# Kernel optimization log

Measured on AMD Instinct MI355X. Metric: run time of the kernel, lower is better.

The kernel has to match this reference:

```python
import jax, jax.numpy as jnp
import numpy as np

NUM_MAPS = 512
NUM_BLOCKS = 2
ZG = 512
HID = min(96, NUM_MAPS)          # shared query / attention hidden dim
SEQ = 8                           # hardcoded inner sequence length
H1 = min(NUM_MAPS // 32, 3)       # num_heads1 = 3
H2 = NUM_MAPS // 32               # num_heads2 = 16
NPROC = NUM_BLOCKS * 4            # 4 FiLM param types per block


def _mha(q, k, v, nheads):
    """Multi-head attention. q:(Lq,D) k,v:(Lk,D) -> (Lq,D)."""
    Lq, D = q.shape
    Lk = k.shape[0]
    d = D // nheads
    qh = q.reshape(Lq, nheads, d).transpose(1, 0, 2)   # (h,Lq,d)
    kh = k.reshape(Lk, nheads, d).transpose(1, 0, 2)
    vh = v.reshape(Lk, nheads, d).transpose(1, 0, 2)
    A = jax.nn.softmax(jnp.einsum('hqd,hkd->hqk', qh, kh) / jnp.sqrt(jnp.asarray(D, q.dtype)))
    O = jnp.einsum('hqk,hkd->hqd', A, vh)
    return O.transpose(1, 0, 2).reshape(Lq, D)


def setup_inputs() -> dict:
    key = jax.random.key(0)
    ks = jax.random.split(key, 20)
    s = 0.05
    n = jax.random.normal
    return {
        'gate': jax.random.uniform(ks[0], (1, SEQ), dtype=jnp.float32),
        'x': n(ks[1], (1, ZG), dtype=jnp.float32),
        # shared_layer_alphaC : Linear(ZG, NUM_MAPS) + Sigmoid
        'Wa': n(ks[2], (ZG, NUM_MAPS)) * s, 'ba': jnp.zeros((NUM_MAPS,)),
        # shared_layer_Query : Linear(ZG, HID) + ReLU
        'Wqr': n(ks[3], (ZG, HID)) * s, 'bqr': jnp.zeros((HID,)),
        # stacked FiLM params: [block, {g1,b1,g2,b2}, num_maps, 8]
        'P': n(ks[4], (NUM_BLOCKS, 4, NUM_MAPS, SEQ)) * 0.2,
        'De': n(ks[5], (NUM_BLOCKS, 4, NUM_MAPS, SEQ)) * 0.01,
        'regs': n(ks[6], (NUM_BLOCKS, 4, NUM_MAPS)) * 0.001,
        # SMAB_small processor weights, stacked over the 8 processors
        'Wq1': n(ks[7], (NPROC, NUM_MAPS, HID)) * s,
        'Wk1': n(ks[8], (NPROC, NUM_MAPS, HID)) * s,
        'Wv1': n(ks[9], (NPROC, NUM_MAPS, HID)) * s,
        'fc1': n(ks[10], (NPROC, HID, HID)) * s,
        'Wq2': n(ks[11], (NPROC, HID, HID)) * s,
        'Wk2': n(ks[12], (NPROC, HID, HID)) * s,
        'Wv2': n(ks[13], (NPROC, HID, HID)) * s,
        'fc2': n(ks[14], (NPROC, HID, HID)) * s,
        'Wo': n(ks[15], (NPROC, HID, NUM_MAPS)) * s,
    }


def reference(gate, x, Wa, ba, Wqr, bqr, P, De, regs,
              Wq1, Wk1, Wv1, fc1, Wq2, Wk2, Wv2, fc2, Wo):
    alpha = jax.nn.sigmoid(x @ Wa + ba).reshape(-1)        # (NUM_MAPS,)
    q = jax.nn.relu(x @ Wqr + bqr)                          # (1, HID)

    # per-processor key/value set: transpose(1,0).view(1,8,num_maps)
    K_all = P.reshape(NPROC, NUM_MAPS, SEQ).transpose(0, 2, 1)  # (8procs, 8, NUM_MAPS)

    def smab(K, wq1, wk1, wv1, f1, wq2, wk2, wv2, f2, wo):
        # stage 1: self-attention over the 8-element set (num_heads1)
        Qk = K @ wq1                                        # (8, HID)
        H = Qk + _mha(Qk, K @ wk1, K @ wv1, H1)
        H = H + jax.nn.relu(H @ f1)
        # stage 2: task query attends to the set (num_heads2)
        Qq = q @ wq2                                        # (1, HID)
        O = Qq + _mha(Qq, H @ wk2, H @ wv2, H2)
        O = O + jax.nn.relu(O @ f2)
        return (O @ wo)[0]                                  # (NUM_MAPS,)

    trans = jax.vmap(smab)(K_all, Wq1, Wk1, Wv1, fc1, Wq2, Wk2, Wv2, fc2, Wo)
    trans = trans.reshape(NUM_BLOCKS, 4, NUM_MAPS)

    de = (De * gate[0]).sum(-1)                             # (NB,4,NUM_MAPS)
    mix = alpha * trans + (1.0 - alpha) * de
    offs = jnp.array([1.0, 0.0, 1.0, 0.0], dtype=mix.dtype).reshape(1, 4, 1)
    # gamma gets +1 offset, beta does not
    return mix * regs + offs
```

## Files before the change

kernel.cpp:

```cpp
#include <hip/hip_runtime.h>
#include <hip/hip_bf16.h>
#include <math.h>


#define WS_ALPHA 0
#define WS_Q     512
#define WS_QKV   608

__global__ __launch_bounds__(256) void k1_qkv_alpha_q(
    const float* __restrict__ x, const float* __restrict__ Wa,
    const float* __restrict__ ba, const float* __restrict__ Wqr,
    const float* __restrict__ bqr, const float* __restrict__ P,
    const float* __restrict__ Wq1, const float* __restrict__ Wk1,
    const float* __restrict__ Wv1, float* __restrict__ ws)
{
    __shared__ float sK[8 * 512];
    __shared__ float sp[256];
    const int blk = blockIdx.x, tid = threadIdx.x;

    if (blk < 288) {
        const int proc = blk / 36, c = blk % 36;
        const float4* P4 = (const float4*)(P + proc * 4096);
        for (int i = tid; i < 1024; i += 256) {
            float4 v = P4[i];
            const int m = i >> 1, off = (i & 1) * 4;
            sK[(off + 0) * 512 + m] = v.x;
            sK[(off + 1) * 512 + m] = v.y;
            sK[(off + 2) * 512 + m] = v.z;
            sK[(off + 3) * 512 + m] = v.w;
        }
        __syncthreads();
        const int rl = tid & 63, qtr = tid >> 6;
        const int r = c * 64 + rl;
        const int mat = r / 768, r2 = r % 768;
        const int s = r2 / 96, h = r2 % 96;
        const float* W = (mat == 0 ? Wq1 : (mat == 1 ? Wk1 : Wv1))
                         + proc * 49152 + (qtr * 128) * 96 + h;
        const float* Ks = sK + s * 512 + qtr * 128;
        float acc = 0.f;
        #pragma unroll 32
        for (int m = 0; m < 128; ++m) acc += Ks[m] * W[m * 96];
        sp[tid] = acc;
        __syncthreads();
        if (qtr == 0) {
            acc = sp[tid] + sp[tid + 64] + sp[tid + 128] + sp[tid + 192];
            ws[WS_QKV + proc * 2304 + r] = acc;
        }
    } else if (blk < 296) {
        for (int k = tid; k < 512; k += 256) sK[k] = x[k];
        __syncthreads();
        const int ml = tid & 63, qtr = tid >> 6;
        const int m = (blk - 288) * 64 + ml;
        const float* W = Wa + (qtr * 128) * 512 + m;
        const float* xq = sK + qtr * 128;
        float acc = 0.f;
        #pragma unroll 32
        for (int k = 0; k < 128; ++k) acc += xq[k] * W[k * 512];
        sp[tid] = acc;
        __syncthreads();
        if (qtr == 0) {
            acc = sp[tid] + sp[tid + 64] + sp[tid + 128] + sp[tid + 192] + ba[m];
            ws[WS_ALPHA + m] = 1.f / (1.f + __expf(-acc));
        }
    } else {
        for (int k = tid; k < 512; k += 256) sK[k] = x[k];
        __syncthreads();
        const int hl = tid & 63, qtr = tid >> 6;
        const int h = (blk - 296) * 64 + hl;
        float acc = 0.f;
        if (h < 96) {
            const float* W = Wqr + (qtr * 128) * 96 + h;
            const float* xq = sK + qtr * 128;
            #pragma unroll 32
            for (int k = 0; k < 128; ++k) acc += xq[k] * W[k * 96];
        }
        sp[tid] = acc;
        __syncthreads();
        if (qtr == 0 && h < 96) {
            acc = sp[tid] + sp[tid + 64] + sp[tid + 128] + sp[tid + 192] + bqr[h];
            ws[WS_Q + h] = fmaxf(acc, 0.f);
        }
    }
}

__global__ __launch_bounds__(512) void k2_attn_out(
    const float* __restrict__ gate, const float* __restrict__ De,
    const float* __restrict__ regs, const float* __restrict__ fc1,
    const float* __restrict__ Wq2, const float* __restrict__ Wk2,
    const float* __restrict__ Wv2, const float* __restrict__ fc2,
    const float* __restrict__ Wo, const float* __restrict__ ws,
    float* __restrict__ out)
{
    const int proc = blockIdx.x, tid = threadIdx.x;
    __shared__ float sQk[768], sKk[768], sVv[768], sH[768], sH2[768];
    __shared__ float sK2[768], sV2[768];
    __shared__ float sq[96], sQq[96], sO[96], sOf[96], sS[192], sg[8];
    const float rs = 0.10206207261596577f;

    const float* qkv = ws + WS_QKV + proc * 2304;
    for (int i = tid; i < 768; i += 512) {
        sQk[i] = qkv[i]; sKk[i] = qkv[768 + i]; sVv[i] = qkv[1536 + i];
    }
    if (tid < 96) sq[tid] = ws[WS_Q + tid];
    if (tid < 8)  sg[tid] = gate[tid];
    __syncthreads();

    if (tid < 192) {
        const int h0 = tid / 64, rem = tid % 64, si = rem / 8, sk = rem % 8;
        float acc = 0.f;
        #pragma unroll
        for (int d = 0; d < 32; ++d)
            acc += sQk[si * 96 + h0 * 32 + d] * sKk[sk * 96 + h0 * 32 + d];
        sS[tid] = acc * rs;
    }
    __syncthreads();

    if (tid < 24) {
        const int h0 = tid / 8, si = tid % 8;
        const float* row = sS + h0 * 64 + si * 8;
        float mx = row[0];
        #pragma unroll
        for (int k = 1; k < 8; ++k) mx = fmaxf(mx, row[k]);
        float e[8], sum = 0.f;
        #pragma unroll
        for (int k = 0; k < 8; ++k) { e[k] = __expf(row[k] - mx); sum += e[k]; }
        const float inv = 1.f / sum;
        #pragma unroll
        for (int d = 0; d < 32; ++d) {
            float o = 0.f;
            #pragma unroll
            for (int k = 0; k < 8; ++k) o += e[k] * sVv[k * 96 + h0 * 32 + d];
            const int idx = si * 96 + h0 * 32 + d;
            sH[idx] = sQk[idx] + o * inv;
        }
    }
    __syncthreads();

    for (int idx = tid; idx < 768; idx += 512) {
        const int s = idx / 96, j = idx % 96;
        const float* W = fc1 + proc * 9216 + j;
        const float* Hs = sH + s * 96;
        float acc = 0.f;
        #pragma unroll 32
        for (int i = 0; i < 96; ++i) acc += Hs[i] * W[i * 96];
        sH2[idx] = sH[idx] + fmaxf(acc, 0.f);
    }
    if (tid < 96) {
        const float* W = Wq2 + proc * 9216 + tid;
        float acc = 0.f;
        #pragma unroll 32
        for (int i = 0; i < 96; ++i) acc += sq[i] * W[i * 96];
        sQq[tid] = acc;
    }
    __syncthreads();

    for (int idx = tid; idx < 1536; idx += 512) {
        const int which = idx / 768, r = idx % 768;
        const int s = r / 96, j = r % 96;
        const float* W = (which ? Wv2 : Wk2) + proc * 9216 + j;
        const float* Hs = sH2 + s * 96;
        float acc = 0.f;
        #pragma unroll 32
        for (int i = 0; i < 96; ++i) acc += Hs[i] * W[i * 96];
        if (which) sV2[r] = acc; else sK2[r] = acc;
    }
    __syncthreads();

    if (tid < 16) {
        const int h0 = tid;
        float lg[8], mx = -1e30f;
        #pragma unroll
        for (int k = 0; k < 8; ++k) {
            float acc = 0.f;
            #pragma unroll
            for (int d = 0; d < 6; ++d)
                acc += sQq[h0 * 6 + d] * sK2[k * 96 + h0 * 6 + d];
            lg[k] = acc * rs; mx = fmaxf(mx, lg[k]);
        }
        float e[8], sum = 0.f;
        #pragma unroll
        for (int k = 0; k < 8; ++k) { e[k] = __expf(lg[k] - mx); sum += e[k]; }
        const float inv = 1.f / sum;
        #pragma unroll
        for (int d = 0; d < 6; ++d) {
            float o = 0.f;
            #pragma unroll
            for (int k = 0; k < 8; ++k) o += e[k] * sV2[k * 96 + h0 * 6 + d];
            sO[h0 * 6 + d] = sQq[h0 * 6 + d] + o * inv;
        }
    }
    __syncthreads();

    if (tid < 96) {
        const float* W = fc2 + proc * 9216 + tid;
        float acc = 0.f;
        #pragma unroll 32
        for (int i = 0; i < 96; ++i) acc += sO[i] * W[i * 96];
        sOf[tid] = sO[tid] + fmaxf(acc, 0.f);
    }
    __syncthreads();

    {
        const int m = tid;
        const float* W = Wo + proc * 49152 + m;
        float tr = 0.f;
        #pragma unroll 32
        for (int h = 0; h < 96; ++h) tr += sOf[h] * W[h * 512];
        const float* Dp = De + proc * 4096 + m * 8;
        float de = 0.f;
        #pragma unroll
        for (int s = 0; s < 8; ++s) de += Dp[s] * sg[s];
        const float a = ws[WS_ALPHA + m];
        const float mix = a * tr + (1.f - a) * de;
        const int pt = proc & 3;
        const float off = (pt == 0 || pt == 2) ? 1.f : 0.f;
        out[proc * 512 + m] = mix * regs[proc * 512 + m] + off;
    }
}

extern "C" void kernel_launch(void* const* d_in, const int* in_sizes, int n_in,
                              void* d_out, int out_size, void* d_ws, size_t ws_size,
                              hipStream_t stream)
{
    const float* gate = (const float*)d_in[0];
    const float* x    = (const float*)d_in[1];
    const float* Wa   = (const float*)d_in[2];
    const float* ba   = (const float*)d_in[3];
    const float* Wqr  = (const float*)d_in[4];
    const float* bqr  = (const float*)d_in[5];
    const float* P    = (const float*)d_in[6];
    const float* De   = (const float*)d_in[7];
    const float* regs = (const float*)d_in[8];
    const float* Wq1  = (const float*)d_in[9];
    const float* Wk1  = (const float*)d_in[10];
    const float* Wv1  = (const float*)d_in[11];
    const float* fc1  = (const float*)d_in[12];
    const float* Wq2  = (const float*)d_in[13];
    const float* Wk2  = (const float*)d_in[14];
    const float* Wv2  = (const float*)d_in[15];
    const float* fc2  = (const float*)d_in[16];
    const float* Wo   = (const float*)d_in[17];
    float* ws = (float*)d_ws;

    hipLaunchKernelGGL(k1_qkv_alpha_q, dim3(298), dim3(256), 0, stream,
                       x, Wa, ba, Wqr, bqr, P, Wq1, Wk1, Wv1, ws);
    hipLaunchKernelGGL(k2_attn_out, dim3(8), dim3(512), 0, stream,
                       gate, De, regs, fc1, Wq2, Wk2, Wv2, fc2, Wo, ws,
                       (float*)d_out);
}
```

Measured before the change: 116.6 us.

## Double k1 grid with 8-way K split and prefetch k2 weights into cache

Measured after the change: 160.0 us. 37.2% more time.

```diff
diff --git a/kernel.cpp b/kernel.cpp
--- a/kernel.cpp
+++ b/kernel.cpp
@@ -18,8 +18,8 @@
     __shared__ float sp[256];
     const int blk = blockIdx.x, tid = threadIdx.x;
 
-    if (blk < 288) {
-        const int proc = blk / 36, c = blk % 36;
+    if (blk < 576) {
+        const int proc = blk / 72, c = blk % 72;
         const float4* P4 = (const float4*)(P + proc * 4096);
         for (int i = tid; i < 1024; i += 256) {
             float4 v = P4[i];
@@ -30,55 +30,59 @@
             sK[(off + 3) * 512 + m] = v.w;
         }
         __syncthreads();
-        const int rl = tid & 63, qtr = tid >> 6;
-        const int r = c * 64 + rl;
+        const int rl = tid & 31, sp8 = tid >> 5;
+        const int r = c * 32 + rl;
         const int mat = r / 768, r2 = r % 768;
         const int s = r2 / 96, h = r2 % 96;
         const float* W = (mat == 0 ? Wq1 : (mat == 1 ? Wk1 : Wv1))
-                         + proc * 49152 + (qtr * 128) * 96 + h;
-        const float* Ks = sK + s * 512 + qtr * 128;
-        float acc = 0.f;
-        #pragma unroll 32
-        for (int m = 0; m < 128; ++m) acc += Ks[m] * W[m * 96];
+                         + proc * 49152 + (sp8 * 64) * 96 + h;
+        const float* Ks = sK + s * 512 + sp8 * 64;
+        float acc = 0.f;
+        #pragma unroll
+        for (int m2 = 0; m2 < 64; ++m2) acc += Ks[m2] * W[m2 * 96];
         sp[tid] = acc;
         __syncthreads();
-        if (qtr == 0) {
-            acc = sp[tid] + sp[tid + 64] + sp[tid + 128] + sp[tid + 192];
-            ws[WS_QKV + proc * 2304 + r] = acc;
-        }
-    } else if (blk < 296) {
+        if (sp8 == 0) {
+            float a = 0.f;
+            #pragma unroll
+            for (int j = 0; j < 8; ++j) a += sp[rl + 32 * j];
+            ws[WS_QKV + proc * 2304 + r] = a;
+        }
+    } else if (blk < 592) {
         for (int k = tid; k < 512; k += 256) sK[k] = x[k];
         __syncthreads();
-        const int ml = tid & 63, qtr = tid >> 6;
-        const int m = (blk - 288) * 64 + ml;
-        const float* W = Wa + (qtr * 128) * 512 + m;
-        const float* xq = sK + qtr * 128;
-        float acc = 0.f;
-        #pragma unroll 32
-        for (int k = 0; k < 128; ++k) acc += xq[k] * W[k * 512];
+        const int ml = tid & 31, sp8 = tid >> 5;
+        const int m = (blk - 576) * 32 + ml;
+        const float* W = Wa + (sp8 * 64) * 512 + m;
+        const float* xq = sK + sp8 * 64;
+        float acc = 0.f;
+        #pragma unroll
+        for (int k = 0; k < 64; ++k) acc += xq[k] * W[k * 512];
         sp[tid] = acc;
         __syncthreads();
-        if (qtr == 0) {
-            acc = sp[tid] + sp[tid + 64] + sp[tid + 128] + sp[tid + 192] + ba[m];
-            ws[WS_ALPHA + m] = 1.f / (1.f + __expf(-acc));
+        if (sp8 == 0) {
+            float a = ba[m];
+            #pragma unroll
+            for (int j = 0; j < 8; ++j) a += sp[ml + 32 * j];
+            ws[WS_ALPHA + m] = 1.f / (1.f + __expf(-a));
         }
     } else {
         for (int k = tid; k < 512; k += 256) sK[k] = x[k];
         __syncthreads();
-        const int hl = tid & 63, qtr = tid >> 6;
-        const int h = (blk - 296) * 64 + hl;
-        float acc = 0.f;
-        if (h < 96) {
-            const float* W = Wqr + (qtr * 128) * 96 + h;
-            const float* xq = sK + qtr * 128;
-            #pragma unroll 32
-            for (int k = 0; k < 128; ++k) acc += xq[k] * W[k * 96];
-        }
+        const int hl = tid & 31, sp8 = tid >> 5;
+        const int h = (blk - 592) * 32 + hl;
+        const float* W = Wqr + (sp8 * 64) * 96 + h;
+        const float* xq = sK + sp8 * 64;
+        float acc = 0.f;
+        #pragma unroll
+        for (int k = 0; k < 64; ++k) acc += xq[k] * W[k * 96];
         sp[tid] = acc;
         __syncthreads();
-        if (qtr == 0 && h < 96) {
-            acc = sp[tid] + sp[tid + 64] + sp[tid + 128] + sp[tid + 192] + bqr[h];
-            ws[WS_Q + h] = fmaxf(acc, 0.f);
+        if (sp8 == 0) {
+            float a = bqr[h];
+            #pragma unroll
+            for (int j = 0; j < 8; ++j) a += sp[hl + 32 * j];
+            ws[WS_Q + h] = fmaxf(a, 0.f);
         }
     }
 }
@@ -88,7 +92,7 @@
     const float* __restrict__ regs, const float* __restrict__ fc1,
     const float* __restrict__ Wq2, const float* __restrict__ Wk2,
     const float* __restrict__ Wv2, const float* __restrict__ fc2,
-    const float* __restrict__ Wo, const float* __restrict__ ws,
+    const float* __restrict__ Wo, float* __restrict__ ws,
     float* __restrict__ out)
 {
     const int proc = blockIdx.x, tid = threadIdx.x;
@@ -97,6 +101,25 @@
     __shared__ float sq[96], sQq[96], sO[96], sOf[96], sS[192], sg[8];
     const float rs = 0.10206207261596577f;
 
+    float dummy = 0.f;
+    {
+        const float2* f1p = (const float2*)(fc1 + proc * 9216) + tid * 9;
+        const float2* q2p = (const float2*)(Wq2 + proc * 9216) + tid * 9;
+        const float2* k2p = (const float2*)(Wk2 + proc * 9216) + tid * 9;
+        const float2* v2p = (const float2*)(Wv2 + proc * 9216) + tid * 9;
+        const float2* f2p = (const float2*)(fc2 + proc * 9216) + tid * 9;
+        #pragma unroll
+        for (int i = 0; i < 9; ++i) {
+            float2 a = f1p[i], b = q2p[i], c = k2p[i], d = v2p[i], e = f2p[i];
+            dummy += a.x + a.y + b.x + b.y + c.x + c.y + d.x + d.y + e.x + e.y;
+        }
+        const float4* wo4 = (const float4*)(Wo + proc * 49152) + tid * 24;
+        #pragma unroll
+        for (int i = 0; i < 24; ++i) {
+            float4 v = wo4[i]; dummy += v.x + v.y + v.z + v.w;
+        }
+    }
+
     const float* qkv = ws + WS_QKV + proc * 2304;
     for (int i = tid; i < 768; i += 512) {
         sQk[i] = qkv[i]; sKk[i] = qkv[768 + i]; sVv[i] = qkv[1536 + i];
@@ -206,16 +229,18 @@
         float tr = 0.f;
         #pragma unroll 32
         for (int h = 0; h < 96; ++h) tr += sOf[h] * W[h * 512];
-        const float* Dp = De + proc * 4096 + m * 8;
-        float de = 0.f;
-        #pragma unroll
-        for (int s = 0; s < 8; ++s) de += Dp[s] * sg[s];
+        const float4* Dp4 = (const float4*)(De + proc * 4096 + m * 8);
+        const float4 d0 = Dp4[0], d1 = Dp4[1];
+        const float de = d0.x * sg[0] + d0.y * sg[1] + d0.z * sg[2] + d0.w * sg[3]
+                       + d1.x * sg[4] + d1.y * sg[5] + d1.z * sg[6] + d1.w * sg[7];
         const float a = ws[WS_ALPHA + m];
         const float mix = a * tr + (1.f - a) * de;
         const int pt = proc & 3;
         const float off = (pt == 0 || pt == 2) ? 1.f : 0.f;
         out[proc * 512 + m] = mix * regs[proc * 512 + m] + off;
     }
+
+    if (dummy != dummy) ws[WS_QKV + proc * 2304] = dummy;
 }
 
 extern "C" void kernel_launch(void* const* d_in, const int* in_sizes, int n_in,
@@ -242,7 +267,7 @@
     const float* Wo   = (const float*)d_in[17];
     float* ws = (float*)d_ws;
 
-    hipLaunchKernelGGL(k1_qkv_alpha_q, dim3(298), dim3(256), 0, stream,
+    hipLaunchKernelGGL(k1_qkv_alpha_q, dim3(595), dim3(256), 0, stream,
                        x, Wa, ba, Wqr, bqr, P, Wq1, Wk1, Wv1, ws);
     hipLaunchKernelGGL(k2_attn_out, dim3(8), dim3(512), 0, stream,
                        gate, De, regs, fc1, Wq2, Wk2, Wv2, fc2, Wo, ws,
```
